# Kernel optimization log

Hardware: AMD Instinct MI355X
Metric: run time of the kernel (lower is better)

## Reference

```python
import jax, jax.numpy as jnp
import numpy as np

B, S, HID = 1, 2048, 3072
NH, NKV, HD = 24, 8, 128
ROT = 96  # partial_rotary_factor 0.75 * head_dim
SCALING = HD ** -0.5
NEG = -1e9


def rotate_half(x):
    x1, x2 = jnp.split(x, 2, axis=-1)
    return jnp.concatenate([-x2, x1], axis=-1)


def setup_inputs() -> dict:
    key = jax.random.key(0)
    ks = jax.random.split(key, 5)
    hidden_states = jax.random.normal(ks[0], (B, S, HID), dtype=jnp.float32)
    # realistic RoPE angles
    inv_freq = 1.0 / (10000.0 ** (jnp.arange(0, ROT, 2, dtype=jnp.float32) / ROT))
    pos = jnp.arange(S, dtype=jnp.float32)
    freqs = pos[:, None] * inv_freq[None, :]              # [S, ROT/2]
    emb = jnp.concatenate([freqs, freqs], axis=-1)        # [S, ROT]
    cos = jnp.cos(emb)[None]                              # [1, S, ROT]
    sin = jnp.sin(emb)[None]
    # additive causal mask [B,1,S,S]
    causal = jnp.tril(jnp.ones((S, S), dtype=bool))
    attention_mask = jnp.where(causal, 0.0, NEG).astype(jnp.float32)[None, None]
    op_size = NH * HD + 2 * NKV * HD
    w_qkv = jax.random.normal(ks[1], (op_size, HID), dtype=jnp.float32) * 0.02
    w_o = jax.random.normal(ks[2], (HID, HID), dtype=jnp.float32) * 0.02
    return {"hidden_states": hidden_states, "cos": cos, "sin": sin,
            "attention_mask": attention_mask, "w_qkv": w_qkv, "w_o": w_o}


def reference(hidden_states, cos, sin, attention_mask, w_qkv, w_o):
    b, s, _ = hidden_states.shape
    qkv = jnp.einsum('bsh,oh->bso', hidden_states, w_qkv)
    q_pos = NH * HD
    k_pos = q_pos + NKV * HD
    q = qkv[..., :q_pos].reshape(b, s, NH, HD).transpose(0, 2, 1, 3)      # [B,NH,S,D]
    k = qkv[..., q_pos:k_pos].reshape(b, s, NKV, HD).transpose(0, 2, 1, 3)  # [B,NKV,S,D]
    v = qkv[..., k_pos:].reshape(b, s, NKV, HD).transpose(0, 2, 1, 3)
    # partial RoPE
    c = cos[:, None]  # [B,1,S,ROT]
    sn = sin[:, None]
    q_rot, q_pass = q[..., :ROT], q[..., ROT:]
    k_rot, k_pass = k[..., :ROT], k[..., ROT:]
    q = jnp.concatenate([q_rot * c + rotate_half(q_rot) * sn, q_pass], axis=-1)
    k = jnp.concatenate([k_rot * c + rotate_half(k_rot) * sn, k_pass], axis=-1)
    # GQA repeat_interleave of KV heads
    n_rep = NH // NKV
    k = jnp.repeat(k, n_rep, axis=1)  # [B,NH,S,D]
    v = jnp.repeat(v, n_rep, axis=1)
    scores = jnp.einsum('bhqd,bhkd->bhqk', q, k) * SCALING
    scores = scores + attention_mask[:, :, :, :k.shape[2]]
    attn_weights = jax.nn.softmax(scores.astype(jnp.float32), axis=-1).astype(q.dtype)
    attn_out = jnp.einsum('bhqk,bhkd->bhqd', attn_weights, v)
    attn_out = attn_out.transpose(0, 2, 1, 3).reshape(b, s, NH * HD)
    out = jnp.einsum('bsh,oh->bso', attn_out, w_o)
    return out, attn_weights
```

## Files before the change

kernel.cpp:

```cpp
#include <hip/hip_runtime.h>
#include <cstdint>
#include <cstddef>

#define S_LEN 2048
#define HID   3072
#define NH    24
#define NKV   8
#define HD    128
#define ROT   96
#define OPSZ  5120
#define NREP  3
#define SCALING 0.08838834764831845f

typedef _Float16 f16;
typedef float f32x4 __attribute__((ext_vector_type(4)));
typedef _Float16 f16x8 __attribute__((ext_vector_type(8)));
typedef _Float16 f16x4 __attribute__((ext_vector_type(4)));

#define GLOBAL_AS __attribute__((address_space(1)))
#define LDS_AS    __attribute__((address_space(3)))

__global__ void k_cast4(const float* __restrict__ in, f16* __restrict__ out, int n4) {
  int i = blockIdx.x * blockDim.x + threadIdx.x;
  if (i >= n4) return;
  float4 v = reinterpret_cast<const float4*>(in)[i];
  f16x4 o = {(f16)v.x, (f16)v.y, (f16)v.z, (f16)v.w};
  reinterpret_cast<f16x4*>(out)[i] = o;
}

__device__ __forceinline__ void stage_async(const f16* __restrict__ G, int ld, int m0, int k0,
                                            f16* __restrict__ Ls) {
  int t = threadIdx.x;
  int lane = t & 63, w = t >> 6;
#pragma unroll
  for (int j = 0; j < 2; ++j) {
    int rowBase = w * 16 + j * 64;
    int row = rowBase + (lane >> 2);
    int seg = lane & 3;
    const f16* gp = G + (size_t)(m0 + row) * ld + k0 + seg * 8;
    f16* lp = Ls + rowBase * 32;
    __builtin_amdgcn_global_load_lds((GLOBAL_AS const void*)gp, (LDS_AS void*)lp, 16, 0, 0);
  }
}

__device__ __forceinline__ void mma_tile(const f16* __restrict__ As, const f16* __restrict__ Bs,
                                         f32x4 acc[4][4], int wm, int wn, int lrow, int quad) {
  f16x8 a[4], b[4];
#pragma unroll
  for (int mi = 0; mi < 4; ++mi)
    a[mi] = *reinterpret_cast<const f16x8*>(As + (wm + mi * 16 + lrow) * 32 + quad * 8);
#pragma unroll
  for (int ni = 0; ni < 4; ++ni)
    b[ni] = *reinterpret_cast<const f16x8*>(Bs + (wn + ni * 16 + lrow) * 32 + quad * 8);
#pragma unroll
  for (int mi = 0; mi < 4; ++mi)
#pragma unroll
    for (int ni = 0; ni < 4; ++ni)
      acc[mi][ni] = __builtin_amdgcn_mfma_f32_16x16x32_f16(a[mi], b[ni], acc[mi][ni], 0, 0, 0);
}

__global__ __launch_bounds__(256) void k_gemm_qkv(const f16* __restrict__ A,
                                                  const f16* __restrict__ B,
                                                  f16* __restrict__ C) {
  int m0 = blockIdx.y * 128, n0 = blockIdx.x * 128;
  __shared__ __align__(16) f16 As[128 * 32];
  __shared__ __align__(16) f16 Bs[128 * 32];
  f32x4 acc[4][4] = {};
  int t = threadIdx.x, lane = t & 63, w = t >> 6;
  int wm = (w >> 1) * 64, wn = (w & 1) * 64, lrow = lane & 15, quad = lane >> 4;
  for (int kb = 0; kb < HID / 32; ++kb) {
    stage_async(A, HID, m0, kb * 32, As);
    stage_async(B, HID, n0, kb * 32, Bs);
    __syncthreads();
    mma_tile(As, Bs, acc, wm, wn, lrow, quad);
    __syncthreads();
  }
#pragma unroll
  for (int mi = 0; mi < 4; ++mi)
#pragma unroll
    for (int ni = 0; ni < 4; ++ni)
#pragma unroll
      for (int r = 0; r < 4; ++r) {
        int row = m0 + wm + mi * 16 + quad * 4 + r;
        int col = n0 + wn + ni * 16 + lrow;
        C[(size_t)row * OPSZ + col] = (f16)acc[mi][ni][r];
      }
}

__global__ __launch_bounds__(256) void k_gemm_out(const f16* __restrict__ A,
                                                  const f16* __restrict__ B,
                                                  float* __restrict__ C) {
  int m0 = blockIdx.y * 128, n0 = blockIdx.x * 128;
  __shared__ __align__(16) f16 As[128 * 32];
  __shared__ __align__(16) f16 Bs[128 * 32];
  f32x4 acc[4][4] = {};
  int t = threadIdx.x, lane = t & 63, w = t >> 6;
  int wm = (w >> 1) * 64, wn = (w & 1) * 64, lrow = lane & 15, quad = lane >> 4;
  for (int kb = 0; kb < HID / 32; ++kb) {
    stage_async(A, HID, m0, kb * 32, As);
    stage_async(B, HID, n0, kb * 32, Bs);
    __syncthreads();
    mma_tile(As, Bs, acc, wm, wn, lrow, quad);
    __syncthreads();
  }
#pragma unroll
  for (int mi = 0; mi < 4; ++mi)
#pragma unroll
    for (int ni = 0; ni < 4; ++ni)
#pragma unroll
      for (int r = 0; r < 4; ++r) {
        int row = m0 + wm + mi * 16 + quad * 4 + r;
        int col = n0 + wn + ni * 16 + lrow;
        C[(size_t)row * HID + col] = acc[mi][ni][r];
      }
}

__global__ void k_rope(const f16* __restrict__ qkv, const float* __restrict__ cosd,
                       const float* __restrict__ sind, f16* __restrict__ Q,
                       f16* __restrict__ Kc) {
  int idx = blockIdx.x * 256 + threadIdx.x;
  int d = idx & 127;
  int s = (idx >> 7) & (S_LEN - 1);
  int hh = idx >> 18;
  int srcCol = (hh < NH) ? hh * HD + d : HID + (hh - NH) * HD + d;
  float x = (float)qkv[(size_t)s * OPSZ + srcCol];
  float r;
  if (d < ROT) {
    float c = cosd[s * ROT + d], sn = sind[s * ROT + d];
    int pd = (d < 48) ? d + 48 : d - 48;
    float px = (float)qkv[(size_t)s * OPSZ + srcCol - d + pd];
    r = x * c + ((d < 48) ? -px : px) * sn;
  } else {
    r = x;
  }
  f16 o = (f16)r;
  if (hh < NH) Q[((size_t)hh * S_LEN + s) * HD + d] = o;
  else         Kc[((size_t)(hh - NH) * S_LEN + s) * HD + d] = o;
}

__global__ void k_vt(const f16* __restrict__ qkv, f16* __restrict__ Vt) {
  __shared__ f16 tile[32][33];
  int s0 = blockIdx.x * 32, d0 = blockIdx.y * 32, kv = blockIdx.z;
  int tx = threadIdx.x & 31, ty = threadIdx.x >> 5;
#pragma unroll
  for (int i = 0; i < 4; ++i)
    tile[ty + i * 8][tx] = qkv[(size_t)(s0 + ty + i * 8) * OPSZ + 4096 + kv * HD + d0 + tx];
  __syncthreads();
#pragma unroll
  for (int i = 0; i < 4; ++i)
    Vt[((size_t)kv * HD + d0 + ty + i * 8) * S_LEN + s0 + tx] = tile[tx][ty + i * 8];
}

__global__ __launch_bounds__(256) void k_scores(const f16* __restrict__ Q,
                                                const f16* __restrict__ Kc,
                                                float* __restrict__ Sc) {
  int bn = blockIdx.x, bm = blockIdx.y, h = blockIdx.z;
  float* out = Sc + (size_t)h * S_LEN * S_LEN;
  int m0 = bm * 128, n0 = bn * 128;
  int t = threadIdx.x;
  if (bn > bm) {
    float4 z = {0.f, 0.f, 0.f, 0.f};
#pragma unroll
    for (int j = 0; j < 16; ++j) {
      int lin = t + 256 * j;
      int row = lin >> 5;
      int seg = lin & 31;
      reinterpret_cast<float4*>(out + (size_t)(m0 + row) * S_LEN + n0)[seg] = z;
    }
    return;
  }
  __shared__ __align__(16) f16 As[128 * 32];
  __shared__ __align__(16) f16 Bs[128 * 32];
  f32x4 acc[4][4] = {};
  const f16* Ah = Q + (size_t)h * S_LEN * HD;
  const f16* Bh = Kc + (size_t)(h / NREP) * S_LEN * HD;
  int lane = t & 63, w = t >> 6;
  int wm = (w >> 1) * 64, wn = (w & 1) * 64, lrow = lane & 15, quad = lane >> 4;
  for (int kb = 0; kb < HD / 32; ++kb) {
    stage_async(Ah, HD, m0, kb * 32, As);
    stage_async(Bh, HD, n0, kb * 32, Bs);
    __syncthreads();
    mma_tile(As, Bs, acc, wm, wn, lrow, quad);
    __syncthreads();
  }
#pragma unroll
  for (int mi = 0; mi < 4; ++mi)
#pragma unroll
    for (int ni = 0; ni < 4; ++ni)
#pragma unroll
      for (int r = 0; r < 4; ++r) {
        int row = m0 + wm + mi * 16 + quad * 4 + r;
        int col = n0 + wn + ni * 16 + lrow;
        float v = acc[mi][ni][r] * SCALING;
        if (col > row) v = 0.f;
        out[(size_t)row * S_LEN + col] = v;
      }
}

__global__ __launch_bounds__(256) void k_softmax(float* __restrict__ Sc) {
  int r = blockIdx.x & (S_LEN - 1);
  int h = blockIdx.x >> 11;
  float* row = Sc + ((size_t)h * S_LEN + r) * S_LEN;
  int n = r + 1;
  int t = threadIdx.x;
  float vals[8];
  int cnt = 0;
  float mx = -3.0e38f;
  for (int i = t; i < n; i += 256) {
    float v = row[i];
    vals[cnt++] = v;
    mx = fmaxf(mx, v);
  }
  __shared__ float red[4];
#pragma unroll
  for (int o = 32; o > 0; o >>= 1) mx = fmaxf(mx, __shfl_down(mx, o));
  if ((t & 63) == 0) red[t >> 6] = mx;
  __syncthreads();
  mx = fmaxf(fmaxf(red[0], red[1]), fmaxf(red[2], red[3]));
  __syncthreads();
  float sum = 0.f;
  for (int j = 0; j < cnt; ++j) {
    vals[j] = __expf(vals[j] - mx);
    sum += vals[j];
  }
#pragma unroll
  for (int o = 32; o > 0; o >>= 1) sum += __shfl_down(sum, o);
  if ((t & 63) == 0) red[t >> 6] = sum;
  __syncthreads();
  sum = red[0] + red[1] + red[2] + red[3];
  float inv = 1.0f / sum;
  cnt = 0;
  for (int i = t; i < n; i += 256) row[i] = vals[cnt++] * inv;
}

__global__ __launch_bounds__(256) void k_pv(const float* __restrict__ Sc,
                                            const f16* __restrict__ Vt,
                                            f16* __restrict__ AO) {
  int bm = blockIdx.x, h = blockIdx.y;
  int m0 = bm * 128;
  const float* P = Sc + (size_t)h * S_LEN * S_LEN;
  const f16* B = Vt + (size_t)(h / NREP) * HD * S_LEN;
  __shared__ __align__(16) f16 As[128 * 32];
  __shared__ __align__(16) f16 Bs[128 * 32];
  f32x4 acc[4][4] = {};
  int t = threadIdx.x, lane = t & 63, w = t >> 6;
  int wm = (w >> 1) * 64, wn = (w & 1) * 64, lrow = lane & 15, quad = lane >> 4;
  int nkb = (bm + 1) * 4;
  for (int kb = 0; kb < nkb; ++kb) {
#pragma unroll
    for (int j = 0; j < 4; ++j) {
      int lin = t + 256 * j;
      int row = lin >> 3, seg = lin & 7;
      float4 v = reinterpret_cast<const float4*>(P + (size_t)(m0 + row) * S_LEN + kb * 32)[seg];
      f16x4 o = {(f16)v.x, (f16)v.y, (f16)v.z, (f16)v.w};
      *reinterpret_cast<f16x4*>(As + row * 32 + seg * 4) = o;
    }
    stage_async(B, S_LEN, 0, kb * 32, Bs);
    __syncthreads();
    mma_tile(As, Bs, acc, wm, wn, lrow, quad);
    __syncthreads();
  }
#pragma unroll
  for (int mi = 0; mi < 4; ++mi)
#pragma unroll
    for (int ni = 0; ni < 4; ++ni)
#pragma unroll
      for (int r = 0; r < 4; ++r) {
        int row = m0 + wm + mi * 16 + quad * 4 + r;
        int col = wn + ni * 16 + lrow;
        AO[(size_t)row * HID + h * HD + col] = (f16)acc[mi][ni][r];
      }
}

extern "C" void kernel_launch(void* const* d_in, const int* in_sizes, int n_in,
                              void* d_out, int out_size, void* d_ws, size_t ws_size,
                              hipStream_t stream) {
  const float* hs    = (const float*)d_in[0];
  const float* cosd  = (const float*)d_in[1];
  const float* sind  = (const float*)d_in[2];
  const float* w_qkv = (const float*)d_in[4];
  const float* w_o   = (const float*)d_in[5];

  float* out  = (float*)d_out;
  float* attn = out + (size_t)S_LEN * HID;

  char* ws = (char*)d_ws;
  f16* hs16   = (f16*)(ws + 0);
  f16* wq16   = (f16*)(ws + 12582912);
  f16* qkv16  = (f16*)(ws + 44040192);
  f16* Q16    = (f16*)(ws + 65011712);
  f16* K16    = (f16*)(ws + 77594624);
  f16* Vt16   = (f16*)(ws + 81788928);
  f16* AO16   = hs16;
  f16* Wo16   = wq16;

  k_cast4<<<6144, 256, 0, stream>>>(hs, hs16, (S_LEN * HID) / 4);
  k_cast4<<<15360, 256, 0, stream>>>(w_qkv, wq16, (OPSZ * HID) / 4);
  k_gemm_qkv<<<dim3(40, 16), 256, 0, stream>>>(hs16, wq16, qkv16);
  k_rope<<<32768, 256, 0, stream>>>(qkv16, cosd, sind, Q16, K16);
  k_vt<<<dim3(64, 4, 8), 256, 0, stream>>>(qkv16, Vt16);
  k_cast4<<<9216, 256, 0, stream>>>(w_o, Wo16, (HID * HID) / 4);
  k_scores<<<dim3(16, 16, 24), 256, 0, stream>>>(Q16, K16, attn);
  k_softmax<<<NH * S_LEN, 256, 0, stream>>>(attn);
  k_pv<<<dim3(16, 24), 256, 0, stream>>>(attn, Vt16, AO16);
  k_gemm_out<<<dim3(24, 16), 256, 0, stream>>>(AO16, Wo16, out);
}
```

Before: 933.5 us.

## Fuse scores, softmax and PV into a two-pass flash-style attention kernel

Replaces the separate scores, softmax and PV kernels with one fused kernel per (head, 128-row query block). The first pass streams K tiles to compute per-row running max and sum. The second pass recomputes scores, writes the normalized probabilities to the attention-weights output, and multiplies them with V from LDS using double-buffered, XOR-swizzled async loads. This removes the fp32 score-matrix read-modify-write round trips through HBM and two kernel launches, at the cost of computing QK^T twice. Query blocks are paired heavy/light to balance the causal work, and the masked upper region is zero-filled inside the same kernel.

```diff
diff --git a/kernel.cpp b/kernel.cpp
--- a/kernel.cpp
+++ b/kernel.cpp
@@ -151,125 +151,250 @@
     Vt[((size_t)kv * HD + d0 + ty + i * 8) * S_LEN + s0 + tx] = tile[tx][ty + i * 8];
 }
 
-__global__ __launch_bounds__(256) void k_scores(const f16* __restrict__ Q,
-                                                const f16* __restrict__ Kc,
-                                                float* __restrict__ Sc) {
-  int bn = blockIdx.x, bm = blockIdx.y, h = blockIdx.z;
-  float* out = Sc + (size_t)h * S_LEN * S_LEN;
-  int m0 = bm * 128, n0 = bn * 128;
-  int t = threadIdx.x;
-  if (bn > bm) {
-    float4 z = {0.f, 0.f, 0.f, 0.f};
+template <int RB, int NR>
+__device__ __forceinline__ void stage_swz(const f16* __restrict__ G, int ld,
+                                          f16* __restrict__ Ls) {
+  constexpr int RPI = 1024 / RB;
+  constexpr int SEGS = RB / 16;
+  constexpr int ISSUES = (NR * RB) / 4096;
+  int t = threadIdx.x, lane = t & 63, w = t >> 6;
+#pragma unroll
+  for (int j = 0; j < ISSUES; ++j) {
+    int rowBase = (w * ISSUES + j) * RPI;
+    int row = rowBase + lane / SEGS;
+    int gseg = (lane % SEGS) ^ (row & 7);
+    const f16* gp = G + (size_t)row * ld + gseg * 8;
+    f16* lp = Ls + rowBase * (RB / 2);
+    __builtin_amdgcn_global_load_lds((GLOBAL_AS const void*)gp, (LDS_AS void*)lp, 16, 0, 0);
+  }
+}
+
+__global__ __launch_bounds__(256, 2) void k_attn(const f16* __restrict__ Q,
+                                                 const f16* __restrict__ Kc,
+                                                 const f16* __restrict__ Vt,
+                                                 float* __restrict__ attn,
+                                                 f16* __restrict__ AO) {
+  __shared__ __align__(16) f16 Ks[64 * 128];
+  __shared__ __align__(16) f16 Vs[2][128 * 64];
+  __shared__ __align__(16) f16 Ps[128 * 64];
+
+  int bx = blockIdx.x;
+  int pairIdx = bx >> 1;
+  int h = pairIdx / 8;
+  int q8 = pairIdx & 7;
+  int bm = (bx & 1) ? q8 : 15 - q8;
+  int m0 = bm * 128;
+  int nt = 2 * (bm + 1);
+
+  const f16* Qh = Q + (size_t)h * S_LEN * HD;
+  const f16* Kh = Kc + (size_t)(h / NREP) * S_LEN * HD;
+  const f16* Vh = Vt + (size_t)(h / NREP) * HD * S_LEN;
+  float* attnH = attn + (size_t)h * S_LEN * S_LEN;
+
+  int t = threadIdx.x, lane = t & 63, w = t >> 6;
+  int wm = (w >> 1) * 64;
+  int wn = (w & 1) * 32;
+  int wn2 = (w & 1) * 64;
+  int lrow = lane & 15, quad = lane >> 4;
+
+  f16x8 qf[4][4];
+#pragma unroll
+  for (int kq = 0; kq < 4; ++kq)
+#pragma unroll
+    for (int mi = 0; mi < 4; ++mi)
+      qf[kq][mi] = *reinterpret_cast<const f16x8*>(
+          Qh + (size_t)(m0 + wm + mi * 16 + lrow) * HD + kq * 32 + quad * 8);
+
+  stage_swz<256, 64>(Kh, HD, Ks);
+
+  float m_run[4][4], l_run[4][4];
+#pragma unroll
+  for (int mi = 0; mi < 4; ++mi)
+#pragma unroll
+    for (int r = 0; r < 4; ++r) { m_run[mi][r] = -1e30f; l_run[mi][r] = 0.f; }
+
+  for (int kb = 0; kb < nt; ++kb) {
+    __syncthreads();
+    f32x4 sacc[4][2] = {};
+    __builtin_amdgcn_s_setprio(1);
+#pragma unroll
+    for (int kq = 0; kq < 4; ++kq) {
+      int kbyte = kq * 64 + quad * 16;
+      f16x8 b[2];
+#pragma unroll
+      for (int ni = 0; ni < 2; ++ni) {
+        int rowb = wn + ni * 16 + lrow;
+        b[ni] = *reinterpret_cast<const f16x8*>(
+            reinterpret_cast<const char*>(Ks) + rowb * 256 + (kbyte ^ ((rowb & 7) << 4)));
+      }
+#pragma unroll
+      for (int mi = 0; mi < 4; ++mi)
+#pragma unroll
+        for (int ni = 0; ni < 2; ++ni)
+          sacc[mi][ni] =
+              __builtin_amdgcn_mfma_f32_16x16x32_f16(qf[kq][mi], b[ni], sacc[mi][ni], 0, 0, 0);
+    }
+    __builtin_amdgcn_s_setprio(0);
+    __syncthreads();
+    if (kb + 1 < nt) {
+      stage_swz<256, 64>(Kh + (size_t)(kb + 1) * 64 * HD, HD, Ks);
+    } else {
+      stage_swz<256, 64>(Kh, HD, Ks);
+      stage_swz<128, 128>(Vh, S_LEN, Vs[0]);
+    }
+    int n0 = kb * 64;
+#pragma unroll
+    for (int mi = 0; mi < 4; ++mi)
+#pragma unroll
+      for (int r = 0; r < 4; ++r) {
+        int rG = m0 + wm + mi * 16 + quad * 4 + r;
+        float sv0, sv1;
+        {
+          int c0 = n0 + wn + lrow;
+          float s0 = sacc[mi][0][r] * SCALING;
+          sv0 = (c0 > rG) ? -1e30f : s0;
+          int c1 = c0 + 16;
+          float s1 = sacc[mi][1][r] * SCALING;
+          sv1 = (c1 > rG) ? -1e30f : s1;
+        }
+        float tmax = fmaxf(sv0, sv1);
+#pragma unroll
+        for (int msk = 8; msk >= 1; msk >>= 1) tmax = fmaxf(tmax, __shfl_xor(tmax, msk));
+        float mold = m_run[mi][r];
+        float mnew = fmaxf(mold, tmax);
+        float psum = __expf(sv0 - mnew) + __expf(sv1 - mnew);
+#pragma unroll
+        for (int msk = 8; msk >= 1; msk >>= 1) psum += __shfl_xor(psum, msk);
+        l_run[mi][r] = l_run[mi][r] * __expf(mold - mnew) + psum;
+        m_run[mi][r] = mnew;
+      }
+  }
+
+  {
+    float* sm = reinterpret_cast<float*>(Ps);
+    float* sl = sm + 256;
+    if (lrow == 0) {
+#pragma unroll
+      for (int mi = 0; mi < 4; ++mi)
+#pragma unroll
+        for (int r = 0; r < 4; ++r) {
+          int rL = wm + mi * 16 + quad * 4 + r;
+          sm[(w & 1) * 128 + rL] = m_run[mi][r];
+          sl[(w & 1) * 128 + rL] = l_run[mi][r];
+        }
+    }
+    __syncthreads();
+#pragma unroll
+    for (int mi = 0; mi < 4; ++mi)
+#pragma unroll
+      for (int r = 0; r < 4; ++r) {
+        int rL = wm + mi * 16 + quad * 4 + r;
+        float ma = sm[rL], mb = sm[128 + rL];
+        float la = sl[rL], lb = sl[128 + rL];
+        float mm = fmaxf(ma, mb);
+        float ll = la * __expf(ma - mm) + lb * __expf(mb - mm);
+        m_run[mi][r] = mm;
+        l_run[mi][r] = 1.0f / ll;
+      }
+  }
+
+  f32x4 oacc[4][4] = {};
+  for (int kb = 0; kb < nt; ++kb) {
+    __syncthreads();
+    f32x4 sacc[4][2] = {};
+    __builtin_amdgcn_s_setprio(1);
+#pragma unroll
+    for (int kq = 0; kq < 4; ++kq) {
+      int kbyte = kq * 64 + quad * 16;
+      f16x8 b[2];
+#pragma unroll
+      for (int ni = 0; ni < 2; ++ni) {
+        int rowb = wn + ni * 16 + lrow;
+        b[ni] = *reinterpret_cast<const f16x8*>(
+            reinterpret_cast<const char*>(Ks) + rowb * 256 + (kbyte ^ ((rowb & 7) << 4)));
+      }
+#pragma unroll
+      for (int mi = 0; mi < 4; ++mi)
+#pragma unroll
+        for (int ni = 0; ni < 2; ++ni)
+          sacc[mi][ni] =
+              __builtin_amdgcn_mfma_f32_16x16x32_f16(qf[kq][mi], b[ni], sacc[mi][ni], 0, 0, 0);
+    }
+    __builtin_amdgcn_s_setprio(0);
+    __syncthreads();
+    if (kb + 1 < nt) {
+      stage_swz<256, 64>(Kh + (size_t)(kb + 1) * 64 * HD, HD, Ks);
+      stage_swz<128, 128>(Vh + (size_t)(kb + 1) * 64, S_LEN, Vs[(kb + 1) & 1]);
+    }
+    int n0 = kb * 64;
+#pragma unroll
+    for (int mi = 0; mi < 4; ++mi)
+#pragma unroll
+      for (int r = 0; r < 4; ++r) {
+        int rL = wm + mi * 16 + quad * 4 + r;
+        float mm = m_run[mi][r], il = l_run[mi][r];
+#pragma unroll
+        for (int ni = 0; ni < 2; ++ni) {
+          int cL = wn + ni * 16 + lrow;
+          int c = n0 + cL;
+          float s = sacc[mi][ni][r] * SCALING;
+          if (c > m0 + rL) s = -1e30f;
+          float p = __expf(s - mm) * il;
+          attnH[(size_t)(m0 + rL) * S_LEN + c] = p;
+          *reinterpret_cast<f16*>(reinterpret_cast<char*>(Ps) + rL * 128 +
+                                  ((cL * 2) ^ ((rL & 7) << 4))) = (f16)p;
+        }
+      }
+    __syncthreads();
+    const f16* Vc = Vs[kb & 1];
+    __builtin_amdgcn_s_setprio(1);
+#pragma unroll
+    for (int kq = 0; kq < 2; ++kq) {
+      int kbyte = kq * 64 + quad * 16;
+      f16x8 a[4], b[4];
+#pragma unroll
+      for (int mi = 0; mi < 4; ++mi) {
+        int rowp = wm + mi * 16 + lrow;
+        a[mi] = *reinterpret_cast<const f16x8*>(
+            reinterpret_cast<const char*>(Ps) + rowp * 128 + (kbyte ^ ((rowp & 7) << 4)));
+      }
+#pragma unroll
+      for (int ni = 0; ni < 4; ++ni) {
+        int rowv = wn2 + ni * 16 + lrow;
+        b[ni] = *reinterpret_cast<const f16x8*>(
+            reinterpret_cast<const char*>(Vc) + rowv * 128 + (kbyte ^ ((rowv & 7) << 4)));
+      }
+#pragma unroll
+      for (int mi = 0; mi < 4; ++mi)
+#pragma unroll
+        for (int ni = 0; ni < 4; ++ni)
+          oacc[mi][ni] =
+              __builtin_amdgcn_mfma_f32_16x16x32_f16(a[mi], b[ni], oacc[mi][ni], 0, 0, 0);
+    }
+    __builtin_amdgcn_s_setprio(0);
+  }
+
+#pragma unroll
+  for (int mi = 0; mi < 4; ++mi)
+#pragma unroll
+    for (int ni = 0; ni < 4; ++ni)
+#pragma unroll
+      for (int r = 0; r < 4; ++r) {
+        int row = m0 + wm + mi * 16 + quad * 4 + r;
+        int col = wn2 + ni * 16 + lrow;
+        AO[(size_t)row * HID + h * HD + col] = (f16)oacc[mi][ni][r];
+      }
+
+  float4 z = {0.f, 0.f, 0.f, 0.f};
+  for (int zt = bm + 1; zt < 16; ++zt) {
+    float* outp = attnH + (size_t)m0 * S_LEN + zt * 128;
 #pragma unroll
     for (int j = 0; j < 16; ++j) {
       int lin = t + 256 * j;
-      int row = lin >> 5;
-      int seg = lin & 31;
-      reinterpret_cast<float4*>(out + (size_t)(m0 + row) * S_LEN + n0)[seg] = z;
-    }
-    return;
-  }
-  __shared__ __align__(16) f16 As[128 * 32];
-  __shared__ __align__(16) f16 Bs[128 * 32];
-  f32x4 acc[4][4] = {};
-  const f16* Ah = Q + (size_t)h * S_LEN * HD;
-  const f16* Bh = Kc + (size_t)(h / NREP) * S_LEN * HD;
-  int lane = t & 63, w = t >> 6;
-  int wm = (w >> 1) * 64, wn = (w & 1) * 64, lrow = lane & 15, quad = lane >> 4;
-  for (int kb = 0; kb < HD / 32; ++kb) {
-    stage_async(Ah, HD, m0, kb * 32, As);
-    stage_async(Bh, HD, n0, kb * 32, Bs);
-    __syncthreads();
-    mma_tile(As, Bs, acc, wm, wn, lrow, quad);
-    __syncthreads();
-  }
-#pragma unroll
-  for (int mi = 0; mi < 4; ++mi)
-#pragma unroll
-    for (int ni = 0; ni < 4; ++ni)
-#pragma unroll
-      for (int r = 0; r < 4; ++r) {
-        int row = m0 + wm + mi * 16 + quad * 4 + r;
-        int col = n0 + wn + ni * 16 + lrow;
-        float v = acc[mi][ni][r] * SCALING;
-        if (col > row) v = 0.f;
-        out[(size_t)row * S_LEN + col] = v;
-      }
-}
-
-__global__ __launch_bounds__(256) void k_softmax(float* __restrict__ Sc) {
-  int r = blockIdx.x & (S_LEN - 1);
-  int h = blockIdx.x >> 11;
-  float* row = Sc + ((size_t)h * S_LEN + r) * S_LEN;
-  int n = r + 1;
-  int t = threadIdx.x;
-  float vals[8];
-  int cnt = 0;
-  float mx = -3.0e38f;
-  for (int i = t; i < n; i += 256) {
-    float v = row[i];
-    vals[cnt++] = v;
-    mx = fmaxf(mx, v);
-  }
-  __shared__ float red[4];
-#pragma unroll
-  for (int o = 32; o > 0; o >>= 1) mx = fmaxf(mx, __shfl_down(mx, o));
-  if ((t & 63) == 0) red[t >> 6] = mx;
-  __syncthreads();
-  mx = fmaxf(fmaxf(red[0], red[1]), fmaxf(red[2], red[3]));
-  __syncthreads();
-  float sum = 0.f;
-  for (int j = 0; j < cnt; ++j) {
-    vals[j] = __expf(vals[j] - mx);
-    sum += vals[j];
-  }
-#pragma unroll
-  for (int o = 32; o > 0; o >>= 1) sum += __shfl_down(sum, o);
-  if ((t & 63) == 0) red[t >> 6] = sum;
-  __syncthreads();
-  sum = red[0] + red[1] + red[2] + red[3];
-  float inv = 1.0f / sum;
-  cnt = 0;
-  for (int i = t; i < n; i += 256) row[i] = vals[cnt++] * inv;
-}
-
-__global__ __launch_bounds__(256) void k_pv(const float* __restrict__ Sc,
-                                            const f16* __restrict__ Vt,
-                                            f16* __restrict__ AO) {
-  int bm = blockIdx.x, h = blockIdx.y;
-  int m0 = bm * 128;
-  const float* P = Sc + (size_t)h * S_LEN * S_LEN;
-  const f16* B = Vt + (size_t)(h / NREP) * HD * S_LEN;
-  __shared__ __align__(16) f16 As[128 * 32];
-  __shared__ __align__(16) f16 Bs[128 * 32];
-  f32x4 acc[4][4] = {};
-  int t = threadIdx.x, lane = t & 63, w = t >> 6;
-  int wm = (w >> 1) * 64, wn = (w & 1) * 64, lrow = lane & 15, quad = lane >> 4;
-  int nkb = (bm + 1) * 4;
-  for (int kb = 0; kb < nkb; ++kb) {
-#pragma unroll
-    for (int j = 0; j < 4; ++j) {
-      int lin = t + 256 * j;
-      int row = lin >> 3, seg = lin & 7;
-      float4 v = reinterpret_cast<const float4*>(P + (size_t)(m0 + row) * S_LEN + kb * 32)[seg];
-      f16x4 o = {(f16)v.x, (f16)v.y, (f16)v.z, (f16)v.w};
-      *reinterpret_cast<f16x4*>(As + row * 32 + seg * 4) = o;
-    }
-    stage_async(B, S_LEN, 0, kb * 32, Bs);
-    __syncthreads();
-    mma_tile(As, Bs, acc, wm, wn, lrow, quad);
-    __syncthreads();
-  }
-#pragma unroll
-  for (int mi = 0; mi < 4; ++mi)
-#pragma unroll
-    for (int ni = 0; ni < 4; ++ni)
-#pragma unroll
-      for (int r = 0; r < 4; ++r) {
-        int row = m0 + wm + mi * 16 + quad * 4 + r;
-        int col = wn + ni * 16 + lrow;
-        AO[(size_t)row * HID + h * HD + col] = (f16)acc[mi][ni][r];
-      }
+      int rowz = lin >> 5, seg = lin & 31;
+      reinterpret_cast<float4*>(outp + (size_t)rowz * S_LEN)[seg] = z;
+    }
+  }
 }
 
 extern "C" void kernel_launch(void* const* d_in, const int* in_sizes, int n_in,
@@ -300,8 +425,6 @@
   k_rope<<<32768, 256, 0, stream>>>(qkv16, cosd, sind, Q16, K16);
   k_vt<<<dim3(64, 4, 8), 256, 0, stream>>>(qkv16, Vt16);
   k_cast4<<<9216, 256, 0, stream>>>(w_o, Wo16, (HID * HID) / 4);
-  k_scores<<<dim3(16, 16, 24), 256, 0, stream>>>(Q16, K16, attn);
-  k_softmax<<<NH * S_LEN, 256, 0, stream>>>(attn);
-  k_pv<<<dim3(16, 24), 256, 0, stream>>>(attn, Vt16, AO16);
+  k_attn<<<384, 256, 0, stream>>>(Q16, K16, Vt16, attn, AO16);
   k_gemm_out<<<dim3(24, 16), 256, 0, stream>>>(AO16, Wo16, out);
 }
```

New measurement: 1.263 ms. +35.3%, slower.
